# Optimization experiments

Measured on AMD Instinct MI355X. Metric: run time of the kernel, lower is better.

Reference implementation:

```python
import jax, jax.numpy as jnp
import numpy as np
import math

V, T, D, N, H, DFF = 32000, 1024, 1024, 6, 16, 4096
DK = D // H
EPS = 1e-6


def setup_inputs() -> dict:
    key = jax.random.key(0)
    ks = jax.random.split(key, 20)
    s = 0.02
    B = 2
    return {
        "idx": jax.random.randint(ks[0], (B, T), 0, V, dtype=jnp.int32),
        "emb": jax.random.normal(ks[1], (V, D), jnp.float32) * s,
        # attention projections, stored [in, out] so y = x @ W
        "Wq": jax.random.normal(ks[2], (N, D, D), jnp.float32) * s,
        "Wk": jax.random.normal(ks[3], (N, D, D), jnp.float32) * s,
        "Wv": jax.random.normal(ks[4], (N, D, D), jnp.float32) * s,
        "Wo": jax.random.normal(ks[5], (N, D, D), jnp.float32) * s,
        "ln1_a": jnp.ones((N, D), jnp.float32),
        "ln1_b": jnp.zeros((N, D), jnp.float32),
        "ln2_a": jnp.ones((N, D), jnp.float32),
        "ln2_b": jnp.zeros((N, D), jnp.float32),
        "W1": jax.random.normal(ks[6], (N, D, DFF), jnp.float32) * s,
        "b1": jnp.zeros((N, DFF), jnp.float32),
        "W2": jax.random.normal(ks[7], (N, DFF, D), jnp.float32) * s,
        "b2": jnp.zeros((N, D), jnp.float32),
        "fnorm_a": jnp.ones((D,), jnp.float32),
        "fnorm_b": jnp.zeros((D,), jnp.float32),
        "Wp": jax.random.normal(ks[8], (D, V), jnp.float32) * s,
        "bp": jnp.zeros((V,), jnp.float32),
    }


def _layernorm(x, a, b):
    # torch .std() uses Bessel correction (ddof=1); denom is (std + eps), not sqrt(var+eps)
    mean = x.mean(axis=-1, keepdims=True)
    std = jnp.std(x, axis=-1, keepdims=True, ddof=1)
    return a * (x - mean) / (std + EPS) + b


def _pos_encoding(t, d):
    pos = jnp.arange(t, dtype=jnp.float32)[:, None]
    div = jnp.exp(jnp.arange(0, d, 2, dtype=jnp.float32) * (-math.log(10000.0) / d))
    pe = jnp.zeros((t, d), jnp.float32)
    pe = pe.at[:, 0::2].set(jnp.sin(pos * div))
    pe = pe.at[:, 1::2].set(jnp.cos(pos * div))
    return pe


def _forward(idx, emb, Wq, Wk, Wv, Wo, ln1_a, ln1_b, ln2_a, ln2_b,
             W1, b1, W2, b2, fnorm_a, fnorm_b, Wp, bp):
    B, Tc = idx.shape
    x = emb[idx] * math.sqrt(D) + _pos_encoding(Tc, D)  # [B,T,D]
    causal = jnp.tril(jnp.ones((Tc, Tc), bool))  # [T,T]

    def block(x, p):
        wq, wk, wv, wo, a1, c1, a2, c2, w1, bb1, w2, bb2 = p
        h_in = _layernorm(x, a1, c1)
        q = (h_in @ wq).reshape(B, Tc, H, DK).transpose(0, 2, 1, 3)
        k = (h_in @ wk).reshape(B, Tc, H, DK).transpose(0, 2, 1, 3)
        v = (h_in @ wv).reshape(B, Tc, H, DK).transpose(0, 2, 1, 3)
        scores = jnp.einsum('bhqd,bhkd->bhqk', q, k) / math.sqrt(DK)
        scores = jnp.where(causal, scores, -1e9)
        attn = jax.nn.softmax(scores, axis=-1)
        o = jnp.einsum('bhqk,bhkd->bhqd', attn, v)
        o = o.transpose(0, 2, 1, 3).reshape(B, Tc, D) @ wo
        x = x + o
        h2 = _layernorm(x, a2, c2)
        ff = jax.nn.relu(h2 @ w1 + bb1) @ w2 + bb2
        x = x + ff
        return x, None

    x, _ = jax.lax.scan(block, x, (Wq, Wk, Wv, Wo, ln1_a, ln1_b, ln2_a, ln2_b, W1, b1, W2, b2))
    x = _layernorm(x, fnorm_a, fnorm_b)
    logits = x @ Wp + bp  # [B,T,V]
    return logits


def reference(idx, emb, Wq, Wk, Wv, Wo, ln1_a, ln1_b, ln2_a, ln2_b,
              W1, b1, W2, b2, fnorm_a, fnorm_b, Wp, bp):
    return _forward(idx, emb, Wq, Wk, Wv, Wo, ln1_a, ln1_b, ln2_a, ln2_b,
                    W1, b1, W2, b2, fnorm_a, fnorm_b, Wp, bp)
```

## Files before the change

### kernel.cpp

```cpp
#include <hip/hip_runtime.h>
#include <hip/hip_bf16.h>
#include <math.h>

#define VOCAB 32000
#define TSEQ 1024
#define DMODEL 1024
#define NLAYERS 6
#define NHEADS 16
#define DFF 4096
#define DKH 64
#define BATCH 2
#define MROWS (BATCH * TSEQ)
#define LN_EPS 1e-6f
#define QKVS 3072

typedef unsigned short u16;
typedef __attribute__((ext_vector_type(8))) short short8v;
typedef __attribute__((ext_vector_type(4))) float f32x4;

#define WAITCNT_VM(N) asm volatile("s_waitcnt vmcnt(" #N ")" ::: "memory")

__device__ __forceinline__ u16 f2bb(float f) {
    __hip_bfloat16 h = __float2bfloat16(f);
    u16 u; __builtin_memcpy(&u, &h, 2); return u;
}

__device__ __forceinline__ void gload16(const void* g, void* l) {
    __builtin_amdgcn_global_load_lds(
        (const __attribute__((address_space(1))) unsigned int*)g,
        (__attribute__((address_space(3))) unsigned int*)l, 16, 0, 0);
}

__global__ void embed_kernel(const int* __restrict__ idx,
                             const float* __restrict__ emb,
                             float* __restrict__ x) {
    int i = blockIdx.x * blockDim.x + threadIdx.x;
    if (i >= MROWS * DMODEL) return;
    int row = i / DMODEL;
    int d = i - row * DMODEL;
    int t = row % TSEQ;
    int tok = idx[row];
    float e = emb[(size_t)tok * DMODEL + d] * 32.0f;
    float freq = expf(-(float)(d & ~1) * (9.210340371976184f / (float)DMODEL));
    float ang = (float)t * freq;
    float pe = (d & 1) ? cosf(ang) : sinf(ang);
    x[i] = e + pe;
}

template<bool OB16>
__global__ void __launch_bounds__(256) ln_kernel(const float* __restrict__ x,
                                                 const float* __restrict__ a,
                                                 const float* __restrict__ b,
                                                 void* __restrict__ yv) {
    __shared__ float red[8];
    int row = blockIdx.x;
    int tid = threadIdx.x;
    float4 v = ((const float4*)(x + (size_t)row * DMODEL))[tid];
    float s = v.x + v.y + v.z + v.w;
    #pragma unroll
    for (int off = 32; off; off >>= 1) s += __shfl_xor(s, off, 64);
    if ((tid & 63) == 0) red[tid >> 6] = s;
    __syncthreads();
    float mean = (red[0] + red[1] + red[2] + red[3]) * (1.0f / DMODEL);
    float dx = v.x - mean, dy = v.y - mean, dz = v.z - mean, dw = v.w - mean;
    float ss = dx * dx + dy * dy + dz * dz + dw * dw;
    #pragma unroll
    for (int off = 32; off; off >>= 1) ss += __shfl_xor(ss, off, 64);
    if ((tid & 63) == 0) red[4 + (tid >> 6)] = ss;
    __syncthreads();
    float var = (red[4] + red[5] + red[6] + red[7]) * (1.0f / (DMODEL - 1));
    float inv = 1.0f / (sqrtf(var) + LN_EPS);
    const float4 a4 = ((const float4*)a)[tid];
    const float4 b4 = ((const float4*)b)[tid];
    float o0 = a4.x * dx * inv + b4.x;
    float o1 = a4.y * dy * inv + b4.y;
    float o2 = a4.z * dz * inv + b4.z;
    float o3 = a4.w * dw * inv + b4.w;
    if (OB16) {
        ushort4 o; o.x = f2bb(o0); o.y = f2bb(o1); o.z = f2bb(o2); o.w = f2bb(o3);
        ((ushort4*)((u16*)yv + (size_t)row * DMODEL))[tid] = o;
    } else {
        float4 o; o.x = o0; o.y = o1; o.z = o2; o.w = o3;
        ((float4*)((float*)yv + (size_t)row * DMODEL))[tid] = o;
    }
}

__global__ void __launch_bounds__(256) convT(const float* __restrict__ in,
                                             u16* __restrict__ out, int K, int N) {
    __shared__ float t[32][33];
    in  += (size_t)blockIdx.z * K * N;
    out += (size_t)blockIdx.z * K * N;
    const int tx = threadIdx.x, ty = threadIdx.y;
    const int n0 = blockIdx.x * 32, k0 = blockIdx.y * 32;
    #pragma unroll
    for (int i = 0; i < 4; ++i)
        t[ty + i * 8][tx] = in[(size_t)(k0 + ty + i * 8) * N + n0 + tx];
    __syncthreads();
    #pragma unroll
    for (int i = 0; i < 4; ++i)
        out[(size_t)(n0 + ty + i * 8) * K + k0 + tx] = f2bb(t[tx][ty + i * 8]);
}

__global__ void __launch_bounds__(256) convQKVO(const float* __restrict__ Wq,
                                                const float* __restrict__ Wk,
                                                const float* __restrict__ Wv,
                                                const float* __restrict__ Wo,
                                                u16* __restrict__ WqkvT,
                                                u16* __restrict__ WoT) {
    __shared__ float t[32][33];
    const int z = blockIdx.z, L = z >> 2, p = z & 3;
    const size_t MM = (size_t)DMODEL * DMODEL;
    const float* in = (p == 0 ? Wq : p == 1 ? Wk : p == 2 ? Wv : Wo) + (size_t)L * MM;
    u16* out = (p < 3) ? (WqkvT + (size_t)L * 3 * MM + (size_t)p * MM)
                       : (WoT + (size_t)L * MM);
    const int tx = threadIdx.x, ty = threadIdx.y;
    const int n0 = blockIdx.x * 32, k0 = blockIdx.y * 32;
    #pragma unroll
    for (int i = 0; i < 4; ++i)
        t[ty + i * 8][tx] = in[(size_t)(k0 + ty + i * 8) * DMODEL + n0 + tx];
    __syncthreads();
    #pragma unroll
    for (int i = 0; i < 4; ++i)
        out[(size_t)(n0 + ty + i * 8) * DMODEL + k0 + tx] = f2bb(t[tx][ty + i * 8]);
}

template<int BMT, bool BIAS, bool RELU, bool RES, bool OB16>
__global__ void __launch_bounds__(256) gemm_mfma(
    const u16* __restrict__ A, const u16* __restrict__ Bt,
    const float* __restrict__ bias, const float* res,
    void* outp, int N, int K)
{
    constexpr int MR = BMT / 32;
    constexpr int AR = BMT / 64;
    __shared__ u16 Alds[3][BMT * 32];
    __shared__ u16 Blds[3][128 * 32];
    const int tid = threadIdx.x;
    const int w = tid >> 6, lane = tid & 63;
    const int wr = w >> 1, wc = w & 1;
    const size_t bm = (size_t)blockIdx.y * BMT;
    const size_t bn = (size_t)blockIdx.x * 128;
    const int srow = (w << 4) + (lane >> 2);
    const int scol = (((lane & 3) ^ ((lane >> 3) & 3)) << 3);
    const int fr = lane & 15, fq = lane >> 4;
    const int aswz = ((fq ^ ((fr >> 1) & 3)) << 3);

    f32x4 acc[MR][4];
    #pragma unroll
    for (int m = 0; m < MR; ++m)
        #pragma unroll
        for (int n = 0; n < 4; ++n)
            acc[m][n] = (f32x4){0.f, 0.f, 0.f, 0.f};

    auto issue = [&](int kt, int buf) {
        const int k0 = kt * 32;
        #pragma unroll
        for (int li = 0; li < AR; ++li)
            gload16(A + (bm + li * 64 + srow) * K + k0 + scol, Alds[buf] + li * 2048 + w * 512);
        #pragma unroll
        for (int li = 0; li < 2; ++li)
            gload16(Bt + (bn + li * 64 + srow) * K + k0 + scol, Blds[buf] + li * 2048 + w * 512);
    };

    const int nt = K / 32;
    issue(0, 0);
    issue(1, 1);
    if constexpr (AR == 2) WAITCNT_VM(4); else WAITCNT_VM(3);
    __builtin_amdgcn_s_barrier();
    __builtin_amdgcn_sched_barrier(0);

    for (int t = 0; t < nt; ++t) {
        const int pf = (t + 2 < nt) ? t + 2 : nt - 1;
        issue(pf, (t + 2) % 3);
        if constexpr (AR == 2) WAITCNT_VM(8); else WAITCNT_VM(6);
        __builtin_amdgcn_s_barrier();
        __builtin_amdgcn_sched_barrier(0);
        const u16* Ab = Alds[t % 3];
        const u16* Bb = Blds[t % 3];
        short8v a[MR], b[4];
        #pragma unroll
        for (int m = 0; m < MR; ++m)
            a[m] = *(const short8v*)(Ab + (wr * (BMT / 2) + m * 16 + fr) * 32 + aswz);
        #pragma unroll
        for (int n = 0; n < 4; ++n)
            b[n] = *(const short8v*)(Bb + (wc * 64 + n * 16 + fr) * 32 + aswz);
        #pragma unroll
        for (int m = 0; m < MR; ++m)
            #pragma unroll
            for (int n = 0; n < 4; ++n)
                acc[m][n] = __builtin_amdgcn_mfma_f32_16x16x32_bf16(a[m], b[n], acc[m][n], 0, 0, 0);
        __builtin_amdgcn_s_barrier();
    }
    WAITCNT_VM(0);

    #pragma unroll
    for (int n = 0; n < 4; ++n) {
        const size_t col = bn + wc * 64 + n * 16 + fr;
        const float bv = BIAS ? bias[col] : 0.f;
        #pragma unroll
        for (int m = 0; m < MR; ++m) {
            #pragma unroll
            for (int r = 0; r < 4; ++r) {
                const size_t row = bm + wr * (BMT / 2) + m * 16 + fq * 4 + r;
                float v = acc[m][n][r] + bv;
                if (RELU) v = fmaxf(v, 0.f);
                if (RES)  v += res[row * N + col];
                if (OB16) ((u16*)outp)[row * N + col] = f2bb(v);
                else      ((float*)outp)[row * N + col] = v;
            }
        }
    }
}

__global__ void __launch_bounds__(256) attn_flash(const u16* __restrict__ qkv,
                                                  u16* __restrict__ o) {
    __shared__ u16 Klds[64 * 64];
    __shared__ u16 Vt[64 * 64];
    __shared__ u16 Plds[4][16 * 72];

    const int tid = threadIdx.x;
    const int w = tid >> 6, lane = tid & 63;
    const int fr = lane & 15, fq = lane >> 4;
    const int qt = gridDim.x - 1 - blockIdx.x;
    const int h = blockIdx.y, b = blockIdx.z;
    const int qbase = qt * 64 + w * 16;
    const size_t rowbase = (size_t)b * TSEQ;
    const int hd = h * DKH;

    const int rk = tid >> 3;
    const int c8 = (tid & 7) << 3;

    const u16* qrow = qkv + (rowbase + qbase + fr) * QKVS + hd;
    const short8v qf0 = *(const short8v*)(qrow + fq * 8);
    const short8v qf1 = *(const short8v*)(qrow + 32 + fq * 8);

    float m[4], l[4];
    f32x4 oa[4];
    #pragma unroll
    for (int r = 0; r < 4; ++r) { m[r] = -1e30f; l[r] = 0.f; }
    #pragma unroll
    for (int nd = 0; nd < 4; ++nd) oa[nd] = (f32x4){0.f, 0.f, 0.f, 0.f};

    short8v ka0, ka1, va0, va1;
    short8v kb0, kb1, vb0, vb1;

    auto load_set = [&](int j0, short8v& k0v, short8v& k1v, short8v& v0v, short8v& v1v) {
        const size_t gk = (rowbase + j0 + rk) * QKVS + hd + c8 + 1024;
        k0v = *(const short8v*)(qkv + gk);
        k1v = *(const short8v*)(qkv + gk + (size_t)32 * QKVS);
        const size_t gv = (rowbase + j0 + 2 * rk) * QKVS + hd + c8 + 2048;
        v0v = *(const short8v*)(qkv + gv);
        v1v = *(const short8v*)(qkv + gv + QKVS);
    };
    auto stage_set = [&](const short8v& k0v, const short8v& k1v,
                         const short8v& v0v, const short8v& v1v) {
        const int kb0b = (rk * 128 + c8 * 2) ^ ((rk & 7) << 4);
        *(short8v*)((char*)Klds + kb0b) = k0v;
        const int r2 = rk + 32;
        const int kb1b = (r2 * 128 + c8 * 2) ^ ((r2 & 7) << 4);
        *(short8v*)((char*)Klds + kb1b) = k1v;
        #pragma unroll
        for (int i = 0; i < 8; ++i) {
            const int vrow = c8 + i;
            const int slot = (((2 * rk) >> 3) + (vrow >> 3)) & 7;
            unsigned int pair = ((unsigned int)(u16)v0v[i]) |
                                (((unsigned int)(u16)v1v[i]) << 16);
            *(unsigned int*)(&Vt[vrow * 64 + slot * 8 + ((2 * rk) & 7)]) = pair;
        }
    };
    auto do_tile = [&](int t) {
        const int j0 = t * 64;
        f32x4 s[4];
        __builtin_amdgcn_s_setprio(1);
        #pragma unroll
        for (int ct = 0; ct < 4; ++ct) {
            const int krow = ct * 16 + fr;
            const int swz = (krow & 7) << 4;
            short8v k0 = *(const short8v*)((char*)Klds + ((krow * 128 + fq * 16) ^ swz));
            short8v k1 = *(const short8v*)((char*)Klds + ((krow * 128 + 64 + fq * 16) ^ swz));
            f32x4 a = (f32x4){0.f, 0.f, 0.f, 0.f};
            a = __builtin_amdgcn_mfma_f32_16x16x32_bf16(qf0, k0, a, 0, 0, 0);
            a = __builtin_amdgcn_mfma_f32_16x16x32_bf16(qf1, k1, a, 0, 0, 0);
            s[ct] = a;
        }
        __builtin_amdgcn_s_setprio(0);

        float c[4];
        #pragma unroll
        for (int r = 0; r < 4; ++r) {
            const int qg = qbase + fq * 4 + r;
            float sv[4];
            #pragma unroll
            for (int ct = 0; ct < 4; ++ct) {
                sv[ct] = s[ct][r] * 0.125f;
                if (j0 + ct * 16 + fr > qg) sv[ct] = -1e30f;
            }
            float mx = fmaxf(fmaxf(sv[0], sv[1]), fmaxf(sv[2], sv[3]));
            mx = fmaxf(mx, __shfl_xor(mx, 1, 64));
            mx = fmaxf(mx, __shfl_xor(mx, 2, 64));
            mx = fmaxf(mx, __shfl_xor(mx, 4, 64));
            mx = fmaxf(mx, __shfl_xor(mx, 8, 64));
            const float mn = fmaxf(m[r], mx);
            c[r] = __expf(m[r] - mn);
            m[r] = mn;
            float p0 = __expf(sv[0] - mn);
            float p1 = __expf(sv[1] - mn);
            float p2 = __expf(sv[2] - mn);
            float p3 = __expf(sv[3] - mn);
            float rs = (p0 + p1) + (p2 + p3);
            rs += __shfl_xor(rs, 1, 64);
            rs += __shfl_xor(rs, 2, 64);
            rs += __shfl_xor(rs, 4, 64);
            rs += __shfl_xor(rs, 8, 64);
            l[r] = l[r] * c[r] + rs;
            u16* prow = &Plds[w][(fq * 4 + r) * 72];
            prow[fr]      = f2bb(p0);
            prow[16 + fr] = f2bb(p1);
            prow[32 + fr] = f2bb(p2);
            prow[48 + fr] = f2bb(p3);
        }
        #pragma unroll
        for (int nd = 0; nd < 4; ++nd)
            #pragma unroll
            for (int r = 0; r < 4; ++r)
                oa[nd][r] *= c[r];
        asm volatile("s_waitcnt lgkmcnt(0)" ::: "memory");
        __builtin_amdgcn_sched_barrier(0);

        __builtin_amdgcn_s_setprio(1);
        #pragma unroll
        for (int ks = 0; ks < 2; ++ks) {
            const short8v pf = *(const short8v*)(&Plds[w][fr * 72 + ks * 32 + fq * 8]);
            #pragma unroll
            for (int nd = 0; nd < 4; ++nd) {
                const int vrow = nd * 16 + fr;
                const int slot = (ks * 4 + fq + (vrow >> 3)) & 7;
                const short8v vf = *(const short8v*)(&Vt[vrow * 64 + slot * 8]);
                oa[nd] = __builtin_amdgcn_mfma_f32_16x16x32_bf16(pf, vf, oa[nd], 0, 0, 0);
            }
        }
        __builtin_amdgcn_s_setprio(0);
    };

    load_set(0, ka0, ka1, va0, va1);
    int t = 0;
    for (;;) {
        stage_set(ka0, ka1, va0, va1);
        __syncthreads();
        if (t < qt) load_set((t + 1) * 64, kb0, kb1, vb0, vb1);
        do_tile(t);
        __syncthreads();
        if (++t > qt) break;
        stage_set(kb0, kb1, vb0, vb1);
        __syncthreads();
        if (t < qt) load_set((t + 1) * 64, ka0, ka1, va0, va1);
        do_tile(t);
        __syncthreads();
        if (++t > qt) break;
    }

    #pragma unroll
    for (int r = 0; r < 4; ++r) {
        const float inv = 1.0f / l[r];
        u16* orow = o + (rowbase + qbase + fq * 4 + r) * DMODEL + hd;
        #pragma unroll
        for (int nd = 0; nd < 4; ++nd)
            orow[nd * 16 + fr] = f2bb(oa[nd][r] * inv);
    }
}

#define FBM 64
#define FBN 64
#define FBK 16
__global__ void __launch_bounds__(256) gemm_f32(
    const float* __restrict__ A, const float* __restrict__ Bw,
    const float* __restrict__ bias, float* outp, int N, int K)
{
    __shared__ float As[FBK][FBM];
    __shared__ float Bs[FBK][FBN];
    const int bm = blockIdx.y * FBM, bn = blockIdx.x * FBN;
    const int tid = threadIdx.x;
    const int tr = (tid >> 4) << 2, tc = (tid & 15) << 2;
    const int am = tid >> 2, ak = (tid & 3) << 2;
    const int bk = tid >> 4, bn4 = (tid & 15) << 2;
    float acc[4][4] = {};
    const float* Ap = A + (size_t)(bm + am) * K + ak;
    const float* Bp = Bw + (size_t)bk * N + bn + bn4;
    for (int k0 = 0; k0 < K; k0 += FBK) {
        float4 av = *(const float4*)(Ap + k0);
        float4 bv = *(const float4*)(Bp + (size_t)k0 * N);
        As[ak + 0][am] = av.x; As[ak + 1][am] = av.y; As[ak + 2][am] = av.z; As[ak + 3][am] = av.w;
        *(float4*)&Bs[bk][bn4] = bv;
        __syncthreads();
        #pragma unroll
        for (int kk = 0; kk < FBK; ++kk) {
            float4 a4 = *(const float4*)&As[kk][tr];
            float4 b4 = *(const float4*)&Bs[kk][tc];
            acc[0][0] += a4.x*b4.x; acc[0][1] += a4.x*b4.y; acc[0][2] += a4.x*b4.z; acc[0][3] += a4.x*b4.w;
            acc[1][0] += a4.y*b4.x; acc[1][1] += a4.y*b4.y; acc[1][2] += a4.y*b4.z; acc[1][3] += a4.y*b4.w;
            acc[2][0] += a4.z*b4.x; acc[2][1] += a4.z*b4.y; acc[2][2] += a4.z*b4.z; acc[2][3] += a4.z*b4.w;
            acc[3][0] += a4.w*b4.x; acc[3][1] += a4.w*b4.y; acc[3][2] += a4.w*b4.z; acc[3][3] += a4.w*b4.w;
        }
        __syncthreads();
    }
    #pragma unroll
    for (int i = 0; i < 4; ++i) {
        int row = bm + tr + i;
        float4 o;
        o.x = acc[i][0] + bias[bn + tc + 0];
        o.y = acc[i][1] + bias[bn + tc + 1];
        o.z = acc[i][2] + bias[bn + tc + 2];
        o.w = acc[i][3] + bias[bn + tc + 3];
        *(float4*)(outp + (size_t)row * N + bn + tc) = o;
    }
}

extern "C" void kernel_launch(void* const* d_in, const int* in_sizes, int n_in,
                              void* d_out, int out_size, void* d_ws, size_t ws_size,
                              hipStream_t stream) {
    const int* idx = (const int*)d_in[0];
    const float* emb = (const float*)d_in[1];
    const float* Wq = (const float*)d_in[2];
    const float* Wk = (const float*)d_in[3];
    const float* Wv = (const float*)d_in[4];
    const float* Wo = (const float*)d_in[5];
    const float* ln1a = (const float*)d_in[6];
    const float* ln1b = (const float*)d_in[7];
    const float* ln2a = (const float*)d_in[8];
    const float* ln2b = (const float*)d_in[9];
    const float* W1 = (const float*)d_in[10];
    const float* b1 = (const float*)d_in[11];
    const float* W2 = (const float*)d_in[12];
    const float* b2 = (const float*)d_in[13];
    const float* fa = (const float*)d_in[14];
    const float* fb = (const float*)d_in[15];
    const float* Wp = (const float*)d_in[16];
    const float* bp = (const float*)d_in[17];
    float* out = (float*)d_out;

    const size_t MD = (size_t)MROWS * DMODEL;
    const size_t MM = (size_t)DMODEL * DMODEL;
    u16* U = (u16*)out;
    u16* qkv = U;
    u16* ob = U + 3 * MD;
    u16* hb = U + 4 * MD;
    float* x = (float*)(U + 5 * MD);
    u16* ff = U + 7 * MD;
    u16* WqkvT = U + 12 * MD;
    u16* WoT = U + 21 * MD;
    u16* W1T = U + 24 * MD;
    u16* W2T = U + 36 * MD;

    const bool pathA = ws_size >= (size_t)68 * 1024 * 1024 + 256;
    u16* WpT = (u16*)d_ws;
    u16* h2b = (u16*)((char*)d_ws + (size_t)64 * 1024 * 1024);
    float* hF = (float*)d_ws;

    dim3 cblk(32, 8);
    convQKVO<<<dim3(32, 32, 24), cblk, 0, stream>>>(Wq, Wk, Wv, Wo, WqkvT, WoT);
    convT<<<dim3(128, 32, 6), cblk, 0, stream>>>(W1, W1T, DMODEL, DFF);
    convT<<<dim3(32, 128, 6), cblk, 0, stream>>>(W2, W2T, DFF, DMODEL);
    if (pathA) convT<<<dim3(1000, 32, 1), cblk, 0, stream>>>(Wp, WpT, DMODEL, VOCAB);

    embed_kernel<<<(MROWS * DMODEL + 255) / 256, 256, 0, stream>>>(idx, emb, x);

    for (int L = 0; L < NLAYERS; ++L) {
        ln_kernel<true><<<MROWS, 256, 0, stream>>>(x, ln1a + (size_t)L * DMODEL, ln1b + (size_t)L * DMODEL, hb);
        gemm_mfma<128, false, false, false, true><<<dim3(24, 16), 256, 0, stream>>>(
            hb, WqkvT + (size_t)L * 3 * MM, nullptr, nullptr, qkv, QKVS, DMODEL);
        attn_flash<<<dim3(TSEQ / 64, NHEADS, BATCH), 256, 0, stream>>>(qkv, ob);
        gemm_mfma<64, false, false, true, false><<<dim3(8, 32), 256, 0, stream>>>(
            ob, WoT + (size_t)L * MM, nullptr, x, x, DMODEL, DMODEL);
        ln_kernel<true><<<MROWS, 256, 0, stream>>>(x, ln2a + (size_t)L * DMODEL, ln2b + (size_t)L * DMODEL, hb);
        gemm_mfma<128, true, true, false, true><<<dim3(32, 16), 256, 0, stream>>>(
            hb, W1T + (size_t)L * DFF * DMODEL, b1 + (size_t)L * DFF, nullptr, ff, DFF, DMODEL);
        gemm_mfma<64, true, false, true, false><<<dim3(8, 32), 256, 0, stream>>>(
            ff, W2T + (size_t)L * DFF * DMODEL, b2 + (size_t)L * DMODEL, x, x, DMODEL, DFF);
    }

    if (pathA) {
        ln_kernel<true><<<MROWS, 256, 0, stream>>>(x, fa, fb, h2b);
        gemm_mfma<128, true, false, false, false><<<dim3(250, 16), 256, 0, stream>>>(
            h2b, WpT, bp, nullptr, out, VOCAB, DMODEL);
    } else {
        ln_kernel<false><<<MROWS, 256, 0, stream>>>(x, fa, fb, hF);
        gemm_f32<<<dim3(VOCAB / FBN, MROWS / FBM), 256, 0, stream>>>(hF, Wp, bp, out, VOCAB, DMODEL);
    }
}
```

Measured before the change: 1.669 ms.

## Add 8-wave 256-row GEMM tile variant for FFN-up and vocab projection

```diff
diff --git a/kernel.cpp b/kernel.cpp
--- a/kernel.cpp
+++ b/kernel.cpp
@@ -124,14 +124,18 @@
         out[(size_t)(n0 + ty + i * 8) * DMODEL + k0 + tx] = f2bb(t[tx][ty + i * 8]);
 }
 
-template<int BMT, bool BIAS, bool RELU, bool RES, bool OB16>
-__global__ void __launch_bounds__(256) gemm_mfma(
+template<int BMT, int WAVES, bool BIAS, bool RELU, bool RES, bool OB16>
+__global__ void __launch_bounds__(WAVES * 64) gemm_mfma(
     const u16* __restrict__ A, const u16* __restrict__ Bt,
     const float* __restrict__ bias, const float* res,
     void* outp, int N, int K)
 {
-    constexpr int MR = BMT / 32;
-    constexpr int AR = BMT / 64;
+    constexpr int WROWS = BMT / (WAVES / 2);
+    constexpr int MR = WROWS / 16;
+    constexpr int SR = WAVES * 16;
+    constexpr int AR = BMT / SR;
+    constexpr int BR = 128 / SR;
+    constexpr int LD = AR + BR;
     __shared__ u16 Alds[3][BMT * 32];
     __shared__ u16 Blds[3][128 * 32];
     const int tid = threadIdx.x;
@@ -155,23 +159,25 @@
         const int k0 = kt * 32;
         #pragma unroll
         for (int li = 0; li < AR; ++li)
-            gload16(A + (bm + li * 64 + srow) * K + k0 + scol, Alds[buf] + li * 2048 + w * 512);
-        #pragma unroll
-        for (int li = 0; li < 2; ++li)
-            gload16(Bt + (bn + li * 64 + srow) * K + k0 + scol, Blds[buf] + li * 2048 + w * 512);
+            gload16(A + (bm + li * SR + srow) * K + k0 + scol,
+                    Alds[buf] + li * (SR * 32) + w * 512);
+        #pragma unroll
+        for (int li = 0; li < BR; ++li)
+            gload16(Bt + (bn + li * SR + srow) * K + k0 + scol,
+                    Blds[buf] + li * (SR * 32) + w * 512);
     };
 
     const int nt = K / 32;
     issue(0, 0);
     issue(1, 1);
-    if constexpr (AR == 2) WAITCNT_VM(4); else WAITCNT_VM(3);
+    if constexpr (LD == 4) WAITCNT_VM(4); else WAITCNT_VM(3);
     __builtin_amdgcn_s_barrier();
     __builtin_amdgcn_sched_barrier(0);
 
     for (int t = 0; t < nt; ++t) {
         const int pf = (t + 2 < nt) ? t + 2 : nt - 1;
         issue(pf, (t + 2) % 3);
-        if constexpr (AR == 2) WAITCNT_VM(8); else WAITCNT_VM(6);
+        if constexpr (LD == 4) WAITCNT_VM(8); else WAITCNT_VM(6);
         __builtin_amdgcn_s_barrier();
         __builtin_amdgcn_sched_barrier(0);
         const u16* Ab = Alds[t % 3];
@@ -179,7 +185,7 @@
         short8v a[MR], b[4];
         #pragma unroll
         for (int m = 0; m < MR; ++m)
-            a[m] = *(const short8v*)(Ab + (wr * (BMT / 2) + m * 16 + fr) * 32 + aswz);
+            a[m] = *(const short8v*)(Ab + (wr * WROWS + m * 16 + fr) * 32 + aswz);
         #pragma unroll
         for (int n = 0; n < 4; ++n)
             b[n] = *(const short8v*)(Bb + (wc * 64 + n * 16 + fr) * 32 + aswz);
@@ -200,7 +206,7 @@
         for (int m = 0; m < MR; ++m) {
             #pragma unroll
             for (int r = 0; r < 4; ++r) {
-                const size_t row = bm + wr * (BMT / 2) + m * 16 + fq * 4 + r;
+                const size_t row = bm + wr * WROWS + m * 16 + fq * 4 + r;
                 float v = acc[m][n][r] + bv;
                 if (RELU) v = fmaxf(v, 0.f);
                 if (RES)  v += res[row * N + col];
@@ -465,21 +471,21 @@
 
     for (int L = 0; L < NLAYERS; ++L) {
         ln_kernel<true><<<MROWS, 256, 0, stream>>>(x, ln1a + (size_t)L * DMODEL, ln1b + (size_t)L * DMODEL, hb);
-        gemm_mfma<128, false, false, false, true><<<dim3(24, 16), 256, 0, stream>>>(
+        gemm_mfma<128, 4, false, false, false, true><<<dim3(24, 16), 256, 0, stream>>>(
             hb, WqkvT + (size_t)L * 3 * MM, nullptr, nullptr, qkv, QKVS, DMODEL);
         attn_flash<<<dim3(TSEQ / 64, NHEADS, BATCH), 256, 0, stream>>>(qkv, ob);
-        gemm_mfma<64, false, false, true, false><<<dim3(8, 32), 256, 0, stream>>>(
+        gemm_mfma<64, 4, false, false, true, false><<<dim3(8, 32), 256, 0, stream>>>(
             ob, WoT + (size_t)L * MM, nullptr, x, x, DMODEL, DMODEL);
         ln_kernel<true><<<MROWS, 256, 0, stream>>>(x, ln2a + (size_t)L * DMODEL, ln2b + (size_t)L * DMODEL, hb);
-        gemm_mfma<128, true, true, false, true><<<dim3(32, 16), 256, 0, stream>>>(
+        gemm_mfma<256, 8, true, true, false, true><<<dim3(32, 8), 512, 0, stream>>>(
             hb, W1T + (size_t)L * DFF * DMODEL, b1 + (size_t)L * DFF, nullptr, ff, DFF, DMODEL);
-        gemm_mfma<64, true, false, true, false><<<dim3(8, 32), 256, 0, stream>>>(
+        gemm_mfma<64, 4, true, false, true, false><<<dim3(8, 32), 256, 0, stream>>>(
             ff, W2T + (size_t)L * DFF * DMODEL, b2 + (size_t)L * DMODEL, x, x, DMODEL, DFF);
     }
 
     if (pathA) {
         ln_kernel<true><<<MROWS, 256, 0, stream>>>(x, fa, fb, h2b);
-        gemm_mfma<128, true, false, false, false><<<dim3(250, 16), 256, 0, stream>>>(
+        gemm_mfma<256, 8, true, false, false, false><<<dim3(250, 8), 512, 0, stream>>>(
             h2b, WpT, bp, nullptr, out, VOCAB, DMODEL);
     } else {
         ln_kernel<false><<<MROWS, 256, 0, stream>>>(x, fa, fb, hF);
```

Result: no change. 1.643 ms (median of 2 runs) (-1.6%).
